# Performance work log

Hardware: AMD Instinct MI355X
Metric: run time of the kernel (lower is better)

## Reference

```python
import jax, jax.numpy as jnp
import numpy as np

B, T, C = 2, 2048, 1024
NH = 16
HS = C // NH          # 64
BD = max(HS // 4, 16) # 16
HORIZON = 64


def setup_inputs() -> dict:
    key = jax.random.key(0)
    ks = jax.random.split(key, 10)
    s = 0.02
    return {
        "x": jax.random.normal(ks[0], (B, T, C), dtype=jnp.float32),
        "W_disp": jax.random.normal(ks[1], (NH * BD, C), dtype=jnp.float32) * s,
        "W_val": jax.random.normal(ks[2], (C, C), dtype=jnp.float32) * s,
        "rel_pos_emb": jax.random.normal(ks[3], (HORIZON, BD), dtype=jnp.float32) * s,
        "strain_fused_w": jax.random.normal(ks[4], (2 * BD, BD), dtype=jnp.float32) * s,
        "strain_fused_b": jnp.zeros((2 * BD,), dtype=jnp.float32),
        "pos_proj_w": jax.random.normal(ks[5], (BD, BD), dtype=jnp.float32) * s,
        "bond_out_w": jax.random.normal(ks[6], (1, BD), dtype=jnp.float32) * s,
        "damage_out_w": jax.random.normal(ks[7], (1, BD), dtype=jnp.float32) * s,
        "damage_out_b": jnp.full((1,), -3.0, dtype=jnp.float32),
        "c_proj_w": jax.random.normal(ks[8], (C, C), dtype=jnp.float32) * s,
    }


def reference(x, W_disp, W_val, rel_pos_emb, strain_fused_w, strain_fused_b,
              pos_proj_w, bond_out_w, damage_out_w, damage_out_b, c_proj_w):
    Bx, Tx, Cx = x.shape
    delta = min(HORIZON, Tx)
    gelu = lambda t: jax.nn.gelu(t, approximate=False)  # torch F.gelu default (erf)

    # projections: (B, nh, T, D)
    disp = (x @ W_disp.T).reshape(Bx, Tx, NH, BD).transpose(0, 2, 1, 3)
    val = (x @ W_val.T).reshape(Bx, Tx, NH, HS).transpose(0, 2, 1, 3)

    pad = ((0, 0), (0, 0), (delta - 1, 0), (0, 0))
    idx = jnp.arange(Tx)[:, None] + jnp.arange(delta)[None, :]  # (T, delta)
    disp_win = jnp.pad(disp, pad)[:, :, idx, :]                 # (B, nh, T, delta, bd)

    strain = disp_win - disp[:, :, :, None, :]                  # (B, nh, T, delta, bd)
    fused = strain @ strain_fused_w.T + strain_fused_b          # (..., 2*bd)
    bond_feats, damage_feats = fused[..., :BD], fused[..., BD:]

    pos_feat = rel_pos_emb[:delta] @ pos_proj_w.T               # (delta, bd)
    bond_logits = (gelu(bond_feats + pos_feat) @ bond_out_w.T)[..., 0]  # (B,nh,T,delta)
    damage = jax.nn.sigmoid((gelu(damage_feats) @ damage_out_w.T)[..., 0] + damage_out_b)
    logits = bond_logits - damage * 10.0

    cmask = (jnp.arange(Tx)[:, None] - delta + 1 + jnp.arange(delta)[None, :]) >= 0
    logits = jnp.where(cmask, logits, -jnp.inf)
    weights = jax.nn.softmax(logits, axis=-1)                   # (B,nh,T,delta)

    val_win = jnp.pad(val, pad)[:, :, idx, :]                   # (B,nh,T,delta,hs)
    out = jnp.einsum('bhtw,bhtwd->bhtd', weights, val_win)      # (B,nh,T,hs)
    out = out.transpose(0, 2, 1, 3).reshape(Bx, Tx, Cx)
    return out @ c_proj_w.T
```

## Files before the change

### kernel.cpp

```cpp
#include <hip/hip_runtime.h>
#include <hip/hip_bf16.h>
#include <math.h>

#define B_ 2
#define T_ 2048
#define C_ 1024
#define NH_ 16
#define HS_ 64
#define BD_ 16
#define DELTA 64
#define K2G 0.3989422804f

typedef __attribute__((ext_vector_type(8))) short bf16x8_t;
typedef __attribute__((ext_vector_type(4))) float f32x4_t;
typedef __attribute__((address_space(1))) const unsigned int GUI;
typedef __attribute__((address_space(3))) unsigned int LUI;

__device__ __forceinline__ unsigned short f2bf(float f) {
    unsigned u = __float_as_uint(f);
    u = u + 0x7fffu + ((u >> 16) & 1u);
    return (unsigned short)(u >> 16);
}
__device__ __forceinline__ float bf2f(unsigned short h) {
    return __uint_as_float(((unsigned)h) << 16);
}
__device__ __forceinline__ float bflo(unsigned u) { return __uint_as_float(u << 16); }
__device__ __forceinline__ float bfhi(unsigned u) { return __uint_as_float(u & 0xffff0000u); }
__device__ __forceinline__ void glds16(const unsigned short* g, unsigned short* l) {
    __builtin_amdgcn_global_load_lds((GUI*)g, (LUI*)l, 16, 0, 0);
}

__global__ __launch_bounds__(256) void prep_kernel(
    const float* __restrict__ x, const float* __restrict__ wval,
    const float* __restrict__ cproj, const float* __restrict__ Wd,
    const float* __restrict__ sfw, const float* __restrict__ rel,
    const float* __restrict__ ppw, const float* __restrict__ sfb,
    const float* __restrict__ bw, const float* __restrict__ dw,
    const float* __restrict__ dob,
    unsigned short* __restrict__ xb, unsigned short* __restrict__ wvalb,
    unsigned short* __restrict__ cprojb, unsigned short* __restrict__ wc,
    float* __restrict__ cbuf2)
{
    const int bid = blockIdx.x;
    if (bid < 6144) {
        const long long NX = (long long)B_*T_*C_;
        const long long NW = (long long)C_*C_;
        long long e = ((long long)bid * 256 + threadIdx.x) * 4;
        const float* src; unsigned short* dst; long long off;
        if (e < NX)            { src = x;     dst = xb;     off = e; }
        else if (e < NX + NW)  { src = wval;  dst = wvalb;  off = e - NX; }
        else                   { src = cproj; dst = cprojb; off = e - NX - NW; }
        float4 v = *(const float4*)(src + off);
        ushort4 o;
        o.x = f2bf(v.x); o.y = f2bf(v.y); o.z = f2bf(v.z); o.w = f2bf(v.w);
        *(ushort4*)(dst + off) = o;
    } else if (bid < 8192) {
        int idx = (bid - 6144) * 256 + threadIdx.x;
        int c = idx & 1023, row = idx >> 10;
        int h = row >> 5, j = row & 31;
        float s = 0.f;
        #pragma unroll
        for (int d = 0; d < 16; ++d) s += sfw[j*16 + d] * Wd[(h*16 + d)*1024 + c];
        wc[idx] = f2bf(s);
    } else {
        int tid = threadIdx.x;
        if (tid < 64) {
            float acc = 0.f;
            for (int j = 0; j < 16; ++j) {
                float c = sfb[j];
                #pragma unroll
                for (int d = 0; d < 16; ++d) c += rel[tid*16 + d] * ppw[j*16 + d];
                acc += bw[j] * fmaf(K2G*c, c, 0.5f*c);
            }
            cbuf2[tid] = acc;
        } else if (tid == 64) {
            float acc = dob[0];
            for (int j = 0; j < 16; ++j) {
                float c = sfb[16 + j];
                acc += dw[j] * fmaf(K2G*c, c, 0.5f*c);
            }
            cbuf2[64] = acc;
        }
    }
}

template<int MODE>
__global__ __launch_bounds__(256, 3) void gemm64(
    const unsigned short* __restrict__ A,
    const unsigned short* __restrict__ Bw,
    float* __restrict__ Cf, unsigned short* __restrict__ Cb1,
    unsigned short* __restrict__ Cb2,
    int M, int N, int K, int nxt)
{
    __shared__ unsigned short As[64*64];
    __shared__ unsigned short Bs[128*64];
    const int nblk = gridDim.x;
    const int bid = blockIdx.x;
    const int l = (bid & 7) * (nblk >> 3) + (bid >> 3);
    const int nb = l % nxt, mb = l / nxt;
    const int m0 = mb * 64, n0 = nb * 128;
    const int tid = threadIdx.x;
    const int lane = tid & 63;
    const int wid = tid >> 6;
    const int waveM = wid >> 1, waveN = wid & 1;
    const int row16 = lane & 15, quad = lane >> 4;
    const int wbase = wid * 512;

    long long gA[2], gB[4];
    #pragma unroll
    for (int q = 0; q < 2; ++q) {
        int c = q*256 + tid, r = c >> 3, col = (c & 7) * 8;
        gA[q] = (long long)(m0 + r) * K + col;
    }
    #pragma unroll
    for (int q = 0; q < 4; ++q) {
        int c = q*256 + tid, r = c >> 3, col = (c & 7) * 8;
        gB[q] = (long long)(n0 + r) * K + col;
    }

    f32x4_t acc[2][4];
    #pragma unroll
    for (int i = 0; i < 2; ++i)
        #pragma unroll
        for (int j = 0; j < 4; ++j) { f32x4_t z = {0.f,0.f,0.f,0.f}; acc[i][j] = z; }

    for (int k0 = 0; k0 < K; k0 += 64) {
        #pragma unroll
        for (int q = 0; q < 2; ++q)
            glds16(A + gA[q] + k0, As + q*2048 + wbase);
        #pragma unroll
        for (int q = 0; q < 4; ++q)
            glds16(Bw + gB[q] + k0, Bs + q*2048 + wbase);
        __syncthreads();
        #pragma unroll
        for (int kk = 0; kk < 2; ++kk) {
            bf16x8_t af[2], bfv[4];
            #pragma unroll
            for (int mt = 0; mt < 2; ++mt)
                af[mt] = *(const bf16x8_t*)(As + (waveM*32 + mt*16 + row16)*64
                                               + (kk*4 + quad)*8);
            #pragma unroll
            for (int nt = 0; nt < 4; ++nt)
                bfv[nt] = *(const bf16x8_t*)(Bs + (waveN*64 + nt*16 + row16)*64
                                                + (kk*4 + quad)*8);
            #pragma unroll
            for (int mt = 0; mt < 2; ++mt)
                #pragma unroll
                for (int nt = 0; nt < 4; ++nt)
                    acc[mt][nt] = __builtin_amdgcn_mfma_f32_16x16x32_bf16(
                        af[mt], bfv[nt], acc[mt][nt], 0, 0, 0);
        }
        __syncthreads();
    }
    #pragma unroll
    for (int mt = 0; mt < 2; ++mt)
        #pragma unroll
        for (int nt = 0; nt < 4; ++nt) {
            int col = n0 + waveN*64 + nt*16 + row16;
            #pragma unroll
            for (int rr = 0; rr < 4; ++rr) {
                int row = m0 + waveM*32 + mt*16 + quad*4 + rr;
                float v = acc[mt][nt][rr];
                if (MODE == 0) {
                    Cf[(long long)row * N + col] = v;
                } else {
                    if (col < 512) Cb1[(long long)row * 512 + col] = f2bf(v);
                    else           Cb2[(long long)row * 1024 + (col - 512)] = f2bf(v);
                }
            }
        }
}

__global__ __launch_bounds__(256, 3) void attn_kernel(
    const unsigned short* __restrict__ projb,
    const unsigned short* __restrict__ valb,
    const float* __restrict__ cbuf2,
    const float* __restrict__ bw,
    const float* __restrict__ dw,
    unsigned short* __restrict__ attb)
{
    __shared__ __align__(16) unsigned char smem[53928];
    unsigned short* projL = (unsigned short*)(smem);
    unsigned short* Qb    = (unsigned short*)(smem + 10160);
    unsigned short* Qd    = (unsigned short*)(smem + 14256);
    unsigned short* wgtA  = (unsigned short*)(smem);
    unsigned short* valL  = (unsigned short*)(smem + 18352);
    unsigned*       SbL   = (unsigned*)(smem + 35248);
    uint2*          TbL   = (uint2*)(smem + 51888);
    float*          smL   = (float*)(smem + 52904);
    const int t0 = blockIdx.x * 64;
    const int h = blockIdx.y, b = blockIdx.z;
    const int tid = threadIdx.x;
    const int lane = tid & 63, wid = tid >> 6;
    const int row16 = lane & 15, quad = lane >> 4;

    for (int e = tid; e < 128*16; e += 256) {
        int ls = e >> 4, d4 = e & 15;
        int s = t0 - 63 + ls;
        ushort4 v = make_ushort4(0, 0, 0, 0);
        if (s >= 0 && ls < 127)
            v = *(const ushort4*)(valb + (long long)(b*T_ + s)*1024 + h*64 + d4*4);
        *(ushort4*)(valL + ls*66 + d4*4) = v;
    }
    for (int e = tid; e < 127*4; e += 256) {
        int r = e >> 2, c = e & 3;
        int s = t0 - 63 + r;
        uint4 v = make_uint4(0, 0, 0, 0);
        if (s >= 0)
            v = *(const uint4*)(projb + (long long)(b*T_ + s)*512 + h*32 + c*8);
        *(uint4*)(projL + r*40 + c*8) = v;
    }
    __syncthreads();

    {
        int r = tid >> 1, hf = tid & 1;
        bf16x8_t ob, od;
        if (r < 127) {
            bf16x8_t vb = *(const bf16x8_t*)(projL + r*40 + hf*8);
            bf16x8_t vd = *(const bf16x8_t*)(projL + r*40 + 16 + hf*8);
            #pragma unroll
            for (int k = 0; k < 8; ++k) {
                int j = hf*8 + k;
                ob[k] = (short)f2bf(bf2f((unsigned short)vb[k]) * bw[j]);
                od[k] = (short)f2bf(bf2f((unsigned short)vd[k]) * dw[j]);
            }
        } else {
            #pragma unroll
            for (int k = 0; k < 8; ++k) { ob[k] = 0; od[k] = 0; }
        }
        *(bf16x8_t*)(Qb + r*16 + hf*8) = ob;
        *(bf16x8_t*)(Qd + r*16 + hf*8) = od;
    }
    if (tid < 127) {
        int r = tid;
        float Lb = 0.f, Db = 0.f, Ld = 0.f, Dd = 0.f;
        #pragma unroll
        for (int g = 0; g < 4; ++g) {
            bf16x8_t v = *(const bf16x8_t*)(projL + r*40 + g*8);
            #pragma unroll
            for (int k = 0; k < 8; ++k) {
                float a = bf2f((unsigned short)v[k]);
                int j = g*8 + k;
                if (j < 16) { float wj = bw[j];     Lb += wj*a; Db += wj*a*a; }
                else        { float wj = dw[j-16];  Ld += wj*a; Dd += wj*a*a; }
            }
        }
        uint2 o;
        o.x = (unsigned)f2bf(Lb) | ((unsigned)f2bf(Db) << 16);
        o.y = (unsigned)f2bf(Ld) | ((unsigned)f2bf(Dd) << 16);
        TbL[r] = o;
    }
    __syncthreads();

    {
        const int trow = 63 + wid*16 + row16;
        bf16x8_t afull = *(const bf16x8_t*)(projL + trow*40 + quad*8);
        const bool loQ = quad < 2;
        #pragma unroll
        for (int ts = 0; ts < 6; ++ts) {
            const int sb = wid*16 + ts*16;
            if (sb >= 128) continue;
            const int srow = sb + row16;
            bf16x8_t qb = *(const bf16x8_t*)(Qb + srow*16 + (quad & 1)*8);
            bf16x8_t qd = *(const bf16x8_t*)(Qd + srow*16 + (quad & 1)*8);
            bf16x8_t b1, b2;
            #pragma unroll
            for (int k = 0; k < 8; ++k) {
                b1[k] = loQ ? qb[k] : (short)0;
                b2[k] = loQ ? (short)0 : qd[k];
            }
            f32x4_t z = {0.f,0.f,0.f,0.f};
            f32x4_t a1 = __builtin_amdgcn_mfma_f32_16x16x32_bf16(afull, b1, z, 0,0,0);
            f32x4_t a2 = __builtin_amdgcn_mfma_f32_16x16x32_bf16(afull, b2, z, 0,0,0);
            #pragma unroll
            for (int rr = 0; rr < 4; ++rr) {
                int t = wid*16 + quad*4 + rr;
                int w = sb + row16 - t;
                if ((unsigned)w < 64u) {
                    unsigned pk = (unsigned)f2bf(a1[rr]) | ((unsigned)f2bf(a2[rr]) << 16);
                    SbL[t*65 + w] = pk;
                }
            }
        }
    }
    float hLbt, DbtR, hLdt, DdtR;
    {
        uint2 tt = TbL[lane + 63];
        hLbt = 0.5f * bflo(tt.x);  DbtR = bfhi(tt.x);
        hLdt = 0.5f * bflo(tt.y);  DdtR = bfhi(tt.y);
    }
    const float damC = cbuf2[64] - hLdt;
    __syncthreads();

    for (int e = tid; e < 1088; e += 256) ((uint4*)wgtA)[e] = make_uint4(0,0,0,0);
    __syncthreads();

    {
        const int base = t0 + lane - 63;
        const int wbA = lane*136 + lane;
        float sm = 0.f;
        #pragma unroll
        for (int it = 0; it < 16; ++it) {
            const int w = __builtin_amdgcn_readfirstlane(wid*16 + it);
            const float cw0 = cbuf2[w];
            uint2 tt = TbL[lane + w];
            unsigned sp = SbL[lane*65 + w];
            float Lbs = bflo(tt.x), Dbs = bfhi(tt.x);
            float Lds = bflo(tt.y), Dds = bfhi(tt.y);
            float S1 = bflo(sp), S2 = bfhi(sp);
            float bond = fmaf(Lbs, 0.5f, cw0) - hLbt;
            float tb = Dbs + DbtR;  tb = fmaf(-2.f, S1, tb);
            bond = fmaf(K2G, tb, bond);
            float dam = fmaf(Lds, 0.5f, damC);
            float td = Dds + DdtR;  td = fmaf(-2.f, S2, td);
            dam = fmaf(K2G, td, dam);
            float sig = __builtin_amdgcn_rcpf(1.f + __expf(-dam));
            float logit = fmaf(-10.f, sig, bond);
            float ex = (base + w >= 0) ? __expf(logit) : 0.f;
            sm += ex;
            wgtA[wbA + w] = f2bf(ex);
        }
        smL[wid*64 + lane] = sm;
    }
    __syncthreads();

    const int waveM = wid >> 1, waveN = wid & 1;
    f32x4_t acc[2][2];
    #pragma unroll
    for (int i = 0; i < 2; ++i)
        #pragma unroll
        for (int j = 0; j < 2; ++j) { f32x4_t z = {0.f,0.f,0.f,0.f}; acc[i][j] = z; }
    #pragma unroll
    for (int kk = 0; kk < 3; ++kk) {
        const int k0 = waveM*32 + kk*32;
        bf16x8_t af[2], bfv[2];
        #pragma unroll
        for (int mt = 0; mt < 2; ++mt)
            af[mt] = *(const bf16x8_t*)(wgtA + (waveM*32 + mt*16 + row16)*136 + k0 + quad*8);
        #pragma unroll
        for (int nt = 0; nt < 2; ++nt) {
            int d = waveN*32 + nt*16 + row16;
            bf16x8_t bv;
            #pragma unroll
            for (int j = 0; j < 8; ++j)
                bv[j] = (short)valL[(k0 + quad*8 + j)*66 + d];
            bfv[nt] = bv;
        }
        #pragma unroll
        for (int mt = 0; mt < 2; ++mt)
            #pragma unroll
            for (int nt = 0; nt < 2; ++nt)
                acc[mt][nt] = __builtin_amdgcn_mfma_f32_16x16x32_bf16(
                    af[mt], bfv[nt], acc[mt][nt], 0, 0, 0);
    }
    #pragma unroll
    for (int mt = 0; mt < 2; ++mt)
        #pragma unroll
        for (int nt = 0; nt < 2; ++nt) {
            int d = waveN*32 + nt*16 + row16;
            #pragma unroll
            for (int rr = 0; rr < 4; ++rr) {
                int trel = waveM*32 + mt*16 + quad*4 + rr;
                float smt = smL[trel] + smL[64 + trel] + smL[128 + trel] + smL[192 + trel];
                float v = acc[mt][nt][rr] * __builtin_amdgcn_rcpf(smt);
                attb[((long long)(b*T_ + t0 + trel))*1024 + h*64 + d] = f2bf(v);
            }
        }
}

extern "C" void kernel_launch(void* const* d_in, const int* in_sizes, int n_in,
                              void* d_out, int out_size, void* d_ws, size_t ws_size,
                              hipStream_t stream) {
    const float* x    = (const float*)d_in[0];
    const float* Wd   = (const float*)d_in[1];
    const float* Wv   = (const float*)d_in[2];
    const float* rel  = (const float*)d_in[3];
    const float* sfw  = (const float*)d_in[4];
    const float* sfb  = (const float*)d_in[5];
    const float* ppw  = (const float*)d_in[6];
    const float* bow  = (const float*)d_in[7];
    const float* dow  = (const float*)d_in[8];
    const float* dob  = (const float*)d_in[9];
    const float* cpw  = (const float*)d_in[10];
    float* out = (float*)d_out;

    char* w = (char*)d_ws;
    unsigned short* xb      = (unsigned short*)(w);
    unsigned short* wcat    = (unsigned short*)(w + 8388608);
    unsigned short* cprojb  = (unsigned short*)(w + 11534336);
    float*          cbuf2   = (float*)         (w + 13631488);
    unsigned short* projb   = (unsigned short*)(w + 13639680);
    unsigned short* valb    = (unsigned short*)(w + 17833984);
    unsigned short* attb    = (unsigned short*)(w + 26222592);

    prep_kernel<<<8193, 256, 0, stream>>>(
        x, Wv, cpw, Wd, sfw, rel, ppw, sfb, bow, dow, dob,
        xb, wcat + 512*1024, cprojb, wcat, cbuf2);
    gemm64<2><<<768, 256, 0, stream>>>(
        xb, wcat, (float*)nullptr, projb, valb, B_*T_, 1536, C_, 12);
    attn_kernel<<<dim3(T_/64, NH_, B_), 256, 0, stream>>>(
        projb, valb, cbuf2, bow, dow, attb);
    gemm64<0><<<512, 256, 0, stream>>>(
        attb, cprojb, out, (unsigned short*)nullptr, (unsigned short*)nullptr,
        B_*T_, C_, C_, 8);
}
```

Baseline: 163.2 us.

## Use 128x128 GEMM tiles for projection and drop a sync in attention

Adds a gemm128 kernel with 128x128 output tiles (4x4 MFMA tiles per wave) and uses it for the fused disp/value projection GEMM, halving the block count. This raises arithmetic intensity and operand reuse per LDS load, at the cost of fewer blocks (384) and lower occupancy on a large-CU GPU. In the attention kernel, Q and the per-row scalar terms are now computed directly from global memory rather than LDS, so one __syncthreads can be removed and the prologue overlaps better with the LDS staging.

```diff
diff --git a/kernel.cpp b/kernel.cpp
--- a/kernel.cpp
+++ b/kernel.cpp
@@ -85,6 +85,88 @@
 }
 
 template<int MODE>
+__global__ __launch_bounds__(256, 2) void gemm128(
+    const unsigned short* __restrict__ A,
+    const unsigned short* __restrict__ Bw,
+    float* __restrict__ Cf, unsigned short* __restrict__ Cb1,
+    unsigned short* __restrict__ Cb2,
+    int M, int N, int K, int nxt)
+{
+    __shared__ unsigned short As[128*64];
+    __shared__ unsigned short Bs[128*64];
+    const int nblk = gridDim.x;
+    const int bid = blockIdx.x;
+    const int l = (bid & 7) * (nblk >> 3) + (bid >> 3);
+    const int nb = l % nxt, mb = l / nxt;
+    const int m0 = mb * 128, n0 = nb * 128;
+    const int tid = threadIdx.x;
+    const int lane = tid & 63;
+    const int wid = tid >> 6;
+    const int waveM = wid >> 1, waveN = wid & 1;
+    const int row16 = lane & 15, quad = lane >> 4;
+    const int wbase = wid * 512;
+
+    long long gA[4], gB[4];
+    #pragma unroll
+    for (int q = 0; q < 4; ++q) {
+        int c = q*256 + tid, r = c >> 3, col = (c & 7) * 8;
+        gA[q] = (long long)(m0 + r) * K + col;
+        gB[q] = (long long)(n0 + r) * K + col;
+    }
+
+    f32x4_t acc[4][4];
+    #pragma unroll
+    for (int i = 0; i < 4; ++i)
+        #pragma unroll
+        for (int j = 0; j < 4; ++j) { f32x4_t z = {0.f,0.f,0.f,0.f}; acc[i][j] = z; }
+
+    for (int k0 = 0; k0 < K; k0 += 64) {
+        #pragma unroll
+        for (int q = 0; q < 4; ++q) {
+            glds16(A  + gA[q] + k0, As + q*2048 + wbase);
+            glds16(Bw + gB[q] + k0, Bs + q*2048 + wbase);
+        }
+        __syncthreads();
+        #pragma unroll
+        for (int kk = 0; kk < 2; ++kk) {
+            bf16x8_t af[4], bfv[4];
+            #pragma unroll
+            for (int mt = 0; mt < 4; ++mt)
+                af[mt] = *(const bf16x8_t*)(As + (waveM*64 + mt*16 + row16)*64
+                                               + (kk*4 + quad)*8);
+            #pragma unroll
+            for (int nt = 0; nt < 4; ++nt)
+                bfv[nt] = *(const bf16x8_t*)(Bs + (waveN*64 + nt*16 + row16)*64
+                                                + (kk*4 + quad)*8);
+            #pragma unroll
+            for (int mt = 0; mt < 4; ++mt)
+                #pragma unroll
+                for (int nt = 0; nt < 4; ++nt)
+                    acc[mt][nt] = __builtin_amdgcn_mfma_f32_16x16x32_bf16(
+                        af[mt], bfv[nt], acc[mt][nt], 0, 0, 0);
+        }
+        __syncthreads();
+    }
+    #pragma unroll
+    for (int mt = 0; mt < 4; ++mt)
+        #pragma unroll
+        for (int nt = 0; nt < 4; ++nt) {
+            int col = n0 + waveN*64 + nt*16 + row16;
+            #pragma unroll
+            for (int rr = 0; rr < 4; ++rr) {
+                int row = m0 + waveM*64 + mt*16 + quad*4 + rr;
+                float v = acc[mt][nt][rr];
+                if (MODE == 0) {
+                    Cf[(long long)row * N + col] = v;
+                } else {
+                    if (col < 512) Cb1[(long long)row * 512 + col] = f2bf(v);
+                    else           Cb2[(long long)row * 1024 + (col - 512)] = f2bf(v);
+                }
+            }
+        }
+}
+
+template<int MODE>
 __global__ __launch_bounds__(256, 3) void gemm64(
     const unsigned short* __restrict__ A,
     const unsigned short* __restrict__ Bw,
@@ -210,14 +292,14 @@
             v = *(const uint4*)(projb + (long long)(b*T_ + s)*512 + h*32 + c*8);
         *(uint4*)(projL + r*40 + c*8) = v;
     }
-    __syncthreads();
-
     {
         int r = tid >> 1, hf = tid & 1;
+        int s = t0 - 63 + r;
         bf16x8_t ob, od;
-        if (r < 127) {
-            bf16x8_t vb = *(const bf16x8_t*)(projL + r*40 + hf*8);
-            bf16x8_t vd = *(const bf16x8_t*)(projL + r*40 + 16 + hf*8);
+        if (r < 127 && s >= 0) {
+            const unsigned short* row = projb + (long long)(b*T_ + s)*512 + h*32;
+            bf16x8_t vb = *(const bf16x8_t*)(row + hf*8);
+            bf16x8_t vd = *(const bf16x8_t*)(row + 16 + hf*8);
             #pragma unroll
             for (int k = 0; k < 8; ++k) {
                 int j = hf*8 + k;
@@ -232,23 +314,26 @@
         *(bf16x8_t*)(Qd + r*16 + hf*8) = od;
     }
     if (tid < 127) {
-        int r = tid;
+        int s = t0 - 63 + tid;
         float Lb = 0.f, Db = 0.f, Ld = 0.f, Dd = 0.f;
-        #pragma unroll
-        for (int g = 0; g < 4; ++g) {
-            bf16x8_t v = *(const bf16x8_t*)(projL + r*40 + g*8);
-            #pragma unroll
-            for (int k = 0; k < 8; ++k) {
-                float a = bf2f((unsigned short)v[k]);
-                int j = g*8 + k;
-                if (j < 16) { float wj = bw[j];     Lb += wj*a; Db += wj*a*a; }
-                else        { float wj = dw[j-16];  Ld += wj*a; Dd += wj*a*a; }
+        if (s >= 0) {
+            const unsigned short* row = projb + (long long)(b*T_ + s)*512 + h*32;
+            #pragma unroll
+            for (int g = 0; g < 4; ++g) {
+                bf16x8_t v = *(const bf16x8_t*)(row + g*8);
+                #pragma unroll
+                for (int k = 0; k < 8; ++k) {
+                    float a = bf2f((unsigned short)v[k]);
+                    int j = g*8 + k;
+                    if (j < 16) { float wj = bw[j];     Lb += wj*a; Db += wj*a*a; }
+                    else        { float wj = dw[j-16];  Ld += wj*a; Dd += wj*a*a; }
+                }
             }
         }
         uint2 o;
         o.x = (unsigned)f2bf(Lb) | ((unsigned)f2bf(Db) << 16);
         o.y = (unsigned)f2bf(Ld) | ((unsigned)f2bf(Dd) << 16);
-        TbL[r] = o;
+        TbL[tid] = o;
     }
     __syncthreads();
 
@@ -396,7 +481,7 @@
     prep_kernel<<<8193, 256, 0, stream>>>(
         x, Wv, cpw, Wd, sfw, rel, ppw, sfb, bow, dow, dob,
         xb, wcat + 512*1024, cprojb, wcat, cbuf2);
-    gemm64<2><<<768, 256, 0, stream>>>(
+    gemm128<2><<<384, 256, 0, stream>>>(
         xb, wcat, (float*)nullptr, projb, valb, B_*T_, 1536, C_, 12);
     attn_kernel<<<dim3(T_/64, NH_, B_), 256, 0, stream>>>(
         projb, valb, cbuf2, bow, dow, attb);
```

Measured after the change: 168.8 us. 1.03x slower.
